# Kernel optimization log

Hardware: AMD Instinct MI355X
Metric: run time of the kernel (lower is better)

The kernel has to match this reference:

```python
import jax, jax.numpy as jnp
import numpy as np

N_NODES = 100000
N_EDGES = 1250000
D_FEAT = 64


def setup_inputs() -> dict:
    key = jax.random.key(0)
    k1, k2, k3 = jax.random.split(key, 3)
    inputs = jax.random.normal(k1, (N_NODES, D_FEAT), dtype=jnp.float32)
    src = jax.random.randint(k2, (N_EDGES,), 0, N_NODES, dtype=jnp.int32)
    dst = jax.random.randint(k3, (N_EDGES,), 0, N_NODES, dtype=jnp.int32)
    return {"inputs": inputs, "src": src, "dst": dst}


def reference(inputs, src, dst):
    # copy_src: message on each edge is the source node's feature -> gather
    msgs = inputs[src]  # [E, d]
    # gcn_reduce: max over mailbox (incoming messages) per destination node
    agg = jax.ops.segment_max(msgs, dst, num_segments=N_NODES)  # [N, d], -inf for empty
    # Nodes receiving no messages keep their original feature (DGL recv semantics)
    indeg = jax.ops.segment_sum(jnp.ones((src.shape[0],), dtype=jnp.int32), dst,
                                num_segments=N_NODES)  # [N]
    v_feature = jnp.where((indeg > 0)[:, None], agg, inputs)  # [N, d]
    return jnp.concatenate([inputs, v_feature], axis=1)  # [N, 2d]
```

## Files before the change

kernel.cpp:

```cpp
#include <hip/hip_runtime.h>
#include <math.h>

#define D_FEAT 64
#define SCAN_BLOCK 1024
#define NG 8
#define NR 8


__global__ void zero_kernel(int* __restrict__ p, int n) {
    int i = blockIdx.x * blockDim.x + threadIdx.x;
    if (i < n) p[i] = 0;
}

__device__ __forceinline__ int block_scan_excl_1024(int v, int* smem16) {
    int lane = threadIdx.x & 63;
    int wid  = threadIdx.x >> 6;
    int x = v;
    #pragma unroll
    for (int d = 1; d < 64; d <<= 1) {
        int t = __shfl_up(x, d, 64);
        if (lane >= d) x += t;
    }
    if (lane == 63) smem16[wid] = x;
    __syncthreads();
    if (wid == 0) {
        int s = (lane < 16) ? smem16[lane] : 0;
        #pragma unroll
        for (int d = 1; d < 16; d <<= 1) {
            int t = __shfl_up(s, d, 64);
            if (lane >= d) s += t;
        }
        if (lane < 16) smem16[lane] = s;
    }
    __syncthreads();
    int base = (wid > 0) ? smem16[wid - 1] : 0;
    return base + x - v;
}


__global__ void count_group_kernel(const int* __restrict__ dst,
                                   int* __restrict__ priv,
                                   int n_nodes, int n_edges, int egroup) {
    int g = blockIdx.x & (NG - 1);
    int c = blockIdx.x >> 3;
    int nchunks = gridDim.x >> 3;
    int ebeg = g * egroup;
    int eend = ebeg + egroup; if (eend > n_edges) eend = n_edges;
    int* cnt = priv + (size_t)g * n_nodes;
    int stride = nchunks * blockDim.x;
    for (int e = ebeg + c * blockDim.x + threadIdx.x; e < eend; e += stride) {
        atomicAdd(&cnt[dst[e]], 1);
    }
}

__global__ void scanA_fused_kernel(int* __restrict__ priv,
                                   int* __restrict__ offsets,
                                   int* __restrict__ blocksums, int n_nodes) {
    __shared__ int smem16[16];
    int i = blockIdx.x * SCAN_BLOCK + threadIdx.x;
    int total = 0;
    if (i < n_nodes) {
        int run = 0;
        #pragma unroll
        for (int g = 0; g < NG; ++g) {
            size_t idx = (size_t)g * n_nodes + i;
            int t = priv[idx];
            priv[idx] = run;
            run += t;
        }
        total = run;
    }
    int excl = block_scan_excl_1024(total, smem16);
    if (i < n_nodes) offsets[i] = excl;
    if (threadIdx.x == SCAN_BLOCK - 1) blocksums[blockIdx.x] = excl + total;
}

__global__ void scanB_kernel(int* __restrict__ blocksums, int nb) {
    __shared__ int smem16[16];
    int v = ((int)threadIdx.x < nb) ? blocksums[threadIdx.x] : 0;
    int e = block_scan_excl_1024(v, smem16);
    if ((int)threadIdx.x < nb) blocksums[threadIdx.x] = e;
}

__global__ void scanC_kernel(int* __restrict__ offsets,
                             const int* __restrict__ blocksums,
                             int n, int n_edges) {
    int i = blockIdx.x * SCAN_BLOCK + threadIdx.x;
    if (i < n) offsets[i] += blocksums[blockIdx.x];
    if (i == 0) offsets[n] = n_edges;
}

__global__ void scatter_rg_kernel(const int* __restrict__ src,
                                  const int* __restrict__ dst,
                                  const int* __restrict__ offsets,
                                  int* __restrict__ priv,
                                  int* __restrict__ sorted_src,
                                  int n_nodes, int n_edges, int egroup,
                                  int nodes_per_range) {
    int r = blockIdx.x & (NR - 1);
    int g = (blockIdx.x >> 3) & (NG - 1);
    int c = blockIdx.x >> 6;
    int nchunks = gridDim.x >> 6;
    int lo = r * nodes_per_range;
    int hi = lo + nodes_per_range;
    int ebeg = g * egroup;
    int eend = ebeg + egroup; if (eend > n_edges) eend = n_edges;
    int* cur = priv + (size_t)g * n_nodes;
    int stride = nchunks * blockDim.x;
    for (int e = ebeg + c * blockDim.x + threadIdx.x; e < eend; e += stride) {
        int d = dst[e];
        if (d >= lo && d < hi) {
            int pos = offsets[d] + atomicAdd(&cur[d], 1);
            sorted_src[pos] = src[e];
        }
    }
}


__global__ void hist_part_kernel(const int* __restrict__ dst,
                                 int* __restrict__ counts,
                                 int n_edges, int nodes_per_range) {
    int r = blockIdx.x & (NR - 1);
    int c = blockIdx.x / NR;
    int nchunks = gridDim.x / NR;
    int lo = r * nodes_per_range;
    int hi = lo + nodes_per_range;
    int stride = nchunks * blockDim.x;
    for (int e = c * blockDim.x + threadIdx.x; e < n_edges; e += stride) {
        int d = dst[e];
        if (d >= lo && d < hi) atomicAdd(&counts[d], 1);
    }
}

__global__ void scanA_plain_kernel(const int* __restrict__ counts,
                                   int* __restrict__ offsets,
                                   int* __restrict__ blocksums, int n) {
    __shared__ int smem16[16];
    int i = blockIdx.x * SCAN_BLOCK + threadIdx.x;
    int v = (i < n) ? counts[i] : 0;
    int e = block_scan_excl_1024(v, smem16);
    if (i < n) offsets[i] = e;
    if (threadIdx.x == SCAN_BLOCK - 1) blocksums[blockIdx.x] = e + v;
}

__global__ void scanC_plain_kernel(int* __restrict__ offsets,
                                   int* __restrict__ cursor,
                                   const int* __restrict__ blocksums,
                                   int n, int n_edges) {
    int i = blockIdx.x * SCAN_BLOCK + threadIdx.x;
    if (i < n) {
        int o = offsets[i] + blocksums[blockIdx.x];
        offsets[i] = o;
        cursor[i] = o;
    }
    if (i == 0) offsets[n] = n_edges;
}

__global__ void scatter_part_kernel(const int* __restrict__ src,
                                    const int* __restrict__ dst,
                                    int* __restrict__ cursor,
                                    int* __restrict__ sorted_src,
                                    int n_edges, int nodes_per_range) {
    int r = blockIdx.x & (NR - 1);
    int c = blockIdx.x / NR;
    int nchunks = gridDim.x / NR;
    int lo = r * nodes_per_range;
    int hi = lo + nodes_per_range;
    int stride = nchunks * blockDim.x;
    for (int e = c * blockDim.x + threadIdx.x; e < n_edges; e += stride) {
        int d = dst[e];
        if (d >= lo && d < hi) {
            int pos = atomicAdd(&cursor[d], 1);
            sorted_src[pos] = src[e];
        }
    }
}


__global__ void pull_max_kernel(const float* __restrict__ inp,
                                const int* __restrict__ offsets,
                                const int* __restrict__ sorted_src,
                                float* __restrict__ out, int n_nodes) {
    int gtid = blockIdx.x * blockDim.x + threadIdx.x;
    int node = gtid >> 6;
    if (node >= n_nodes) return;
    int lane = threadIdx.x & 63;
    int g = lane >> 4;
    int l = lane & 15;

    int beg = offsets[node];
    int end = offsets[node + 1];

    const float4* inp4 = reinterpret_cast<const float4*>(inp);
    float4 own = inp4[(size_t)node * 16 + l];

    float4 m;
    m.x = -INFINITY; m.y = -INFINITY; m.z = -INFINITY; m.w = -INFINITY;
    int j = beg + g;
    for (; j + 4 < end; j += 8) {
        int s0 = sorted_src[j];
        int s1 = sorted_src[j + 4];
        float4 v0 = inp4[(size_t)s0 * 16 + l];
        float4 v1 = inp4[(size_t)s1 * 16 + l];
        m.x = fmaxf(m.x, fmaxf(v0.x, v1.x));
        m.y = fmaxf(m.y, fmaxf(v0.y, v1.y));
        m.z = fmaxf(m.z, fmaxf(v0.z, v1.z));
        m.w = fmaxf(m.w, fmaxf(v0.w, v1.w));
    }
    if (j < end) {
        int s = sorted_src[j];
        float4 v = inp4[(size_t)s * 16 + l];
        m.x = fmaxf(m.x, v.x);
        m.y = fmaxf(m.y, v.y);
        m.z = fmaxf(m.z, v.z);
        m.w = fmaxf(m.w, v.w);
    }
    m.x = fmaxf(m.x, __shfl_xor(m.x, 16, 64));
    m.y = fmaxf(m.y, __shfl_xor(m.y, 16, 64));
    m.z = fmaxf(m.z, __shfl_xor(m.z, 16, 64));
    m.w = fmaxf(m.w, __shfl_xor(m.w, 16, 64));
    m.x = fmaxf(m.x, __shfl_xor(m.x, 32, 64));
    m.y = fmaxf(m.y, __shfl_xor(m.y, 32, 64));
    m.z = fmaxf(m.z, __shfl_xor(m.z, 32, 64));
    m.w = fmaxf(m.w, __shfl_xor(m.w, 32, 64));

    if (beg == end) m = own;

    float4* out4 = reinterpret_cast<float4*>(out);
    if (lane < 16) {
        out4[(size_t)node * 32 + l] = own;
    } else if (lane < 32) {
        out4[(size_t)node * 32 + 16 + l] = m;
    }
}


extern "C" void kernel_launch(void* const* d_in, const int* in_sizes, int n_in,
                              void* d_out, int out_size, void* d_ws, size_t ws_size,
                              hipStream_t stream) {
    const float* inp = (const float*)d_in[0];
    const int* src = (const int*)d_in[1];
    const int* dst = (const int*)d_in[2];
    float* out = (float*)d_out;

    int n_nodes = in_sizes[0] / D_FEAT;
    int n_edges = in_sizes[1];

    int nScanBlocks = (n_nodes + SCAN_BLOCK - 1) / SCAN_BLOCK;
    int nodes_per_range = (n_nodes + NR - 1) / NR;
    int egroup = (n_edges + NG - 1) / NG;

    int* ws = (int*)d_ws;
    size_t need_main = ((size_t)NG * n_nodes + (size_t)(n_nodes + 1) +
                        (size_t)nScanBlocks + (size_t)n_edges) * sizeof(int);

    if (ws_size >= need_main) {
        int* priv = ws;
        int* offsets = ws + (size_t)NG * n_nodes;
        int* blocksums = offsets + n_nodes + 1;
        int* sorted_src = blocksums + nScanBlocks;

        {
            int total = NG * n_nodes;
            zero_kernel<<<(total + 255) / 256, 256, 0, stream>>>(priv, total);
        }
        count_group_kernel<<<NG * 64, 256, 0, stream>>>(dst, priv, n_nodes,
                                                        n_edges, egroup);
        scanA_fused_kernel<<<nScanBlocks, SCAN_BLOCK, 0, stream>>>(priv, offsets,
                                                                   blocksums, n_nodes);
        scanB_kernel<<<1, SCAN_BLOCK, 0, stream>>>(blocksums, nScanBlocks);
        scanC_kernel<<<nScanBlocks, SCAN_BLOCK, 0, stream>>>(offsets, blocksums,
                                                             n_nodes, n_edges);
        scatter_rg_kernel<<<NR * NG * 20, 256, 0, stream>>>(src, dst, offsets,
                                                            priv, sorted_src,
                                                            n_nodes, n_edges,
                                                            egroup, nodes_per_range);
        {
            int total = n_nodes * 64;
            pull_max_kernel<<<(total + 255) / 256, 256, 0, stream>>>(
                inp, offsets, sorted_src, out, n_nodes);
        }
    } else {
        int* counts_cursor = ws;
        int* offsets = ws + n_nodes;
        int* blocksums = offsets + n_nodes + 1;
        int* sorted_src = blocksums + nScanBlocks;

        zero_kernel<<<(n_nodes + 255) / 256, 256, 0, stream>>>(counts_cursor, n_nodes);
        hist_part_kernel<<<NR * 160, 256, 0, stream>>>(dst, counts_cursor,
                                                       n_edges, nodes_per_range);
        scanA_plain_kernel<<<nScanBlocks, SCAN_BLOCK, 0, stream>>>(counts_cursor,
                                                                   offsets, blocksums,
                                                                   n_nodes);
        scanB_kernel<<<1, SCAN_BLOCK, 0, stream>>>(blocksums, nScanBlocks);
        scanC_plain_kernel<<<nScanBlocks, SCAN_BLOCK, 0, stream>>>(offsets,
                                                                   counts_cursor,
                                                                   blocksums,
                                                                   n_nodes, n_edges);
        scatter_part_kernel<<<NR * 160, 256, 0, stream>>>(src, dst, counts_cursor,
                                                          sorted_src, n_edges,
                                                          nodes_per_range);
        {
            int total = n_nodes * 64;
            pull_max_kernel<<<(total + 255) / 256, 256, 0, stream>>>(
                inp, offsets, sorted_src, out, n_nodes);
        }
    }
}
```

Baseline: 244.7 us.

## Replace three-pass scan with single-pass decoupled lookback scan and memset

Merges the three scan kernels (block scan, block-sum scan, add-back) into one single-pass scan that uses a ticket counter and decoupled lookback over per-tile status words. The zeroing kernel becomes a hipMemsetAsync that also clears the ticket and state array. Grid sizes of the count and scatter kernels are increased. This removes two kernel launches and a pass over the offsets, at the cost of a serial lookback spin on thread 0 of each tile.

```diff
diff --git a/kernel.cpp b/kernel.cpp
--- a/kernel.cpp
+++ b/kernel.cpp
@@ -2,15 +2,10 @@
 #include <math.h>
 
 #define D_FEAT 64
-#define SCAN_BLOCK 1024
 #define NG 8
 #define NR 8
-
-
-__global__ void zero_kernel(int* __restrict__ p, int n) {
-    int i = blockIdx.x * blockDim.x + threadIdx.x;
-    if (i < n) p[i] = 0;
-}
+#define MAXTILES 1024
+
 
 __device__ __forceinline__ int block_scan_excl_1024(int v, int* smem16) {
     int lane = threadIdx.x & 63;
@@ -53,42 +48,86 @@
     }
 }
 
-__global__ void scanA_fused_kernel(int* __restrict__ priv,
-                                   int* __restrict__ offsets,
-                                   int* __restrict__ blocksums, int n_nodes) {
+__global__ void hist_part_kernel(const int* __restrict__ dst,
+                                 int* __restrict__ counts,
+                                 int n_edges, int nodes_per_range) {
+    int r = blockIdx.x & (NR - 1);
+    int c = blockIdx.x / NR;
+    int nchunks = gridDim.x / NR;
+    int lo = r * nodes_per_range;
+    int hi = lo + nodes_per_range;
+    int stride = nchunks * blockDim.x;
+    for (int e = c * blockDim.x + threadIdx.x; e < n_edges; e += stride) {
+        int d = dst[e];
+        if (d >= lo && d < hi) atomicAdd(&counts[d], 1);
+    }
+}
+
+
+__global__ void scan_lookback_kernel(int* __restrict__ priv,
+                                     int* __restrict__ counts,
+                                     int* __restrict__ offsets,
+                                     unsigned long long* __restrict__ states,
+                                     int* __restrict__ ticket,
+                                     int n_nodes, int n_edges, int ntiles) {
     __shared__ int smem16[16];
-    int i = blockIdx.x * SCAN_BLOCK + threadIdx.x;
+    __shared__ int s_tile, s_prefix, s_btotal;
+    int tid = threadIdx.x;
+    if (tid == 0) s_tile = atomicAdd(ticket, 1);
+    __syncthreads();
+    int tile = s_tile;
+    int i = tile * 1024 + tid;
+
     int total = 0;
     if (i < n_nodes) {
-        int run = 0;
-        #pragma unroll
-        for (int g = 0; g < NG; ++g) {
-            size_t idx = (size_t)g * n_nodes + i;
-            int t = priv[idx];
-            priv[idx] = run;
-            run += t;
-        }
-        total = run;
+        if (priv != nullptr) {
+            int run = 0;
+            #pragma unroll
+            for (int g = 0; g < NG; ++g) {
+                size_t idx = (size_t)g * n_nodes + i;
+                int t = priv[idx];
+                priv[idx] = run;
+                run += t;
+            }
+            total = run;
+        } else {
+            total = counts[i];
+        }
     }
     int excl = block_scan_excl_1024(total, smem16);
-    if (i < n_nodes) offsets[i] = excl;
-    if (threadIdx.x == SCAN_BLOCK - 1) blocksums[blockIdx.x] = excl + total;
-}
-
-__global__ void scanB_kernel(int* __restrict__ blocksums, int nb) {
-    __shared__ int smem16[16];
-    int v = ((int)threadIdx.x < nb) ? blocksums[threadIdx.x] : 0;
-    int e = block_scan_excl_1024(v, smem16);
-    if ((int)threadIdx.x < nb) blocksums[threadIdx.x] = e;
-}
-
-__global__ void scanC_kernel(int* __restrict__ offsets,
-                             const int* __restrict__ blocksums,
-                             int n, int n_edges) {
-    int i = blockIdx.x * SCAN_BLOCK + threadIdx.x;
-    if (i < n) offsets[i] += blocksums[blockIdx.x];
-    if (i == 0) offsets[n] = n_edges;
-}
+    if (tid == 1023) s_btotal = excl + total;
+    __syncthreads();
+    int btotal = s_btotal;
+
+    if (tid == 0) {
+        if (tile == 0) {
+            atomicExch(&states[0], (2ULL << 62) | (unsigned long long)btotal);
+            s_prefix = 0;
+        } else {
+            atomicExch(&states[tile], (1ULL << 62) | (unsigned long long)btotal);
+            int pref = 0;
+            int t = tile - 1;
+            while (t >= 0) {
+                unsigned long long st = atomicAdd(&states[t], 0ULL);
+                unsigned long long f = st >> 62;
+                if (f == 2ULL) { pref += (int)(st & 0x3FFFFFFFFFFFFFFFULL); break; }
+                if (f == 1ULL) { pref += (int)(st & 0x3FFFFFFFFFFFFFFFULL); --t; }
+            }
+            atomicExch(&states[tile],
+                       (2ULL << 62) | (unsigned long long)(pref + btotal));
+            s_prefix = pref;
+        }
+    }
+    __syncthreads();
+    int bp = s_prefix;
+    if (i < n_nodes) {
+        int o = bp + excl;
+        offsets[i] = o;
+        if (priv == nullptr) counts[i] = o;
+    }
+    if (tid == 0 && tile == ntiles - 1) offsets[n_nodes] = bp + btotal;
+}
+
 
 __global__ void scatter_rg_kernel(const int* __restrict__ src,
                                   const int* __restrict__ dst,
@@ -116,46 +155,6 @@
     }
 }
 
-
-__global__ void hist_part_kernel(const int* __restrict__ dst,
-                                 int* __restrict__ counts,
-                                 int n_edges, int nodes_per_range) {
-    int r = blockIdx.x & (NR - 1);
-    int c = blockIdx.x / NR;
-    int nchunks = gridDim.x / NR;
-    int lo = r * nodes_per_range;
-    int hi = lo + nodes_per_range;
-    int stride = nchunks * blockDim.x;
-    for (int e = c * blockDim.x + threadIdx.x; e < n_edges; e += stride) {
-        int d = dst[e];
-        if (d >= lo && d < hi) atomicAdd(&counts[d], 1);
-    }
-}
-
-__global__ void scanA_plain_kernel(const int* __restrict__ counts,
-                                   int* __restrict__ offsets,
-                                   int* __restrict__ blocksums, int n) {
-    __shared__ int smem16[16];
-    int i = blockIdx.x * SCAN_BLOCK + threadIdx.x;
-    int v = (i < n) ? counts[i] : 0;
-    int e = block_scan_excl_1024(v, smem16);
-    if (i < n) offsets[i] = e;
-    if (threadIdx.x == SCAN_BLOCK - 1) blocksums[blockIdx.x] = e + v;
-}
-
-__global__ void scanC_plain_kernel(int* __restrict__ offsets,
-                                   int* __restrict__ cursor,
-                                   const int* __restrict__ blocksums,
-                                   int n, int n_edges) {
-    int i = blockIdx.x * SCAN_BLOCK + threadIdx.x;
-    if (i < n) {
-        int o = offsets[i] + blocksums[blockIdx.x];
-        offsets[i] = o;
-        cursor[i] = o;
-    }
-    if (i == 0) offsets[n] = n_edges;
-}
-
 __global__ void scatter_part_kernel(const int* __restrict__ src,
                                     const int* __restrict__ dst,
                                     int* __restrict__ cursor,
@@ -246,32 +245,33 @@
     int n_nodes = in_sizes[0] / D_FEAT;
     int n_edges = in_sizes[1];
 
-    int nScanBlocks = (n_nodes + SCAN_BLOCK - 1) / SCAN_BLOCK;
+    int ntiles = (n_nodes + 1023) / 1024;
     int nodes_per_range = (n_nodes + NR - 1) / NR;
     int egroup = (n_edges + NG - 1) / NG;
 
-    int* ws = (int*)d_ws;
-    size_t need_main = ((size_t)NG * n_nodes + (size_t)(n_nodes + 1) +
-                        (size_t)nScanBlocks + (size_t)n_edges) * sizeof(int);
+    char* base = (char*)d_ws;
+    int* ticket = (int*)base;
+    unsigned long long* states = (unsigned long long*)(base + 8);
+    int* after = (int*)(base + 8 + 8 * MAXTILES);
+    size_t head_bytes = 8 + 8 * (size_t)MAXTILES;
+
+    size_t need_main = head_bytes +
+        ((size_t)NG * n_nodes + (size_t)(n_nodes + 1) + (size_t)n_edges) * sizeof(int);
 
     if (ws_size >= need_main) {
-        int* priv = ws;
-        int* offsets = ws + (size_t)NG * n_nodes;
-        int* blocksums = offsets + n_nodes + 1;
-        int* sorted_src = blocksums + nScanBlocks;
-
-        {
-            int total = NG * n_nodes;
-            zero_kernel<<<(total + 255) / 256, 256, 0, stream>>>(priv, total);
-        }
-        count_group_kernel<<<NG * 64, 256, 0, stream>>>(dst, priv, n_nodes,
-                                                        n_edges, egroup);
-        scanA_fused_kernel<<<nScanBlocks, SCAN_BLOCK, 0, stream>>>(priv, offsets,
-                                                                   blocksums, n_nodes);
-        scanB_kernel<<<1, SCAN_BLOCK, 0, stream>>>(blocksums, nScanBlocks);
-        scanC_kernel<<<nScanBlocks, SCAN_BLOCK, 0, stream>>>(offsets, blocksums,
-                                                             n_nodes, n_edges);
-        scatter_rg_kernel<<<NR * NG * 20, 256, 0, stream>>>(src, dst, offsets,
+        int* priv = after;
+        int* offsets = priv + (size_t)NG * n_nodes;
+        int* sorted_src = offsets + n_nodes + 1;
+
+        size_t zero_bytes = head_bytes + (size_t)NG * n_nodes * sizeof(int);
+        hipMemsetAsync(d_ws, 0, zero_bytes, stream);
+
+        count_group_kernel<<<NG * 256, 256, 0, stream>>>(dst, priv, n_nodes,
+                                                         n_edges, egroup);
+        scan_lookback_kernel<<<ntiles, 1024, 0, stream>>>(priv, nullptr, offsets,
+                                                          states, ticket,
+                                                          n_nodes, n_edges, ntiles);
+        scatter_rg_kernel<<<NR * NG * 32, 256, 0, stream>>>(src, dst, offsets,
                                                             priv, sorted_src,
                                                             n_nodes, n_edges,
                                                             egroup, nodes_per_range);
@@ -281,23 +281,19 @@
                 inp, offsets, sorted_src, out, n_nodes);
         }
     } else {
-        int* counts_cursor = ws;
-        int* offsets = ws + n_nodes;
-        int* blocksums = offsets + n_nodes + 1;
-        int* sorted_src = blocksums + nScanBlocks;
-
-        zero_kernel<<<(n_nodes + 255) / 256, 256, 0, stream>>>(counts_cursor, n_nodes);
-        hist_part_kernel<<<NR * 160, 256, 0, stream>>>(dst, counts_cursor,
-                                                       n_edges, nodes_per_range);
-        scanA_plain_kernel<<<nScanBlocks, SCAN_BLOCK, 0, stream>>>(counts_cursor,
-                                                                   offsets, blocksums,
-                                                                   n_nodes);
-        scanB_kernel<<<1, SCAN_BLOCK, 0, stream>>>(blocksums, nScanBlocks);
-        scanC_plain_kernel<<<nScanBlocks, SCAN_BLOCK, 0, stream>>>(offsets,
-                                                                   counts_cursor,
-                                                                   blocksums,
-                                                                   n_nodes, n_edges);
-        scatter_part_kernel<<<NR * 160, 256, 0, stream>>>(src, dst, counts_cursor,
+        int* counts = after;
+        int* offsets = counts + n_nodes;
+        int* sorted_src = offsets + n_nodes + 1;
+
+        size_t zero_bytes = head_bytes + (size_t)n_nodes * sizeof(int);
+        hipMemsetAsync(d_ws, 0, zero_bytes, stream);
+
+        hist_part_kernel<<<NR * 256, 256, 0, stream>>>(dst, counts, n_edges,
+                                                       nodes_per_range);
+        scan_lookback_kernel<<<ntiles, 1024, 0, stream>>>(nullptr, counts, offsets,
+                                                          states, ticket,
+                                                          n_nodes, n_edges, ntiles);
+        scatter_part_kernel<<<NR * 256, 256, 0, stream>>>(src, dst, counts,
                                                           sorted_src, n_edges,
                                                           nodes_per_range);
         {
```

Result: slower. 251.6 us (+2.9%).
